# Kernel optimization log

Hardware: AMD Instinct MI355X
Metric: run time of the kernel (lower is better)

Reference implementation:

```python
import jax, jax.numpy as jnp
import numpy as np

N_NODES = 50000
N_EDGES = 800000
NUM_GRAPHS = 64
D_IN = 128
D_HID = 128
D_OUT = 1
SLOPE = 0.01  # default leaky_relu negative slope


def setup_inputs() -> dict:
    key = jax.random.key(0)
    ks = jax.random.split(key, 8)
    x = jax.random.normal(ks[0], (N_NODES, D_IN), dtype=jnp.float32)
    edge_index = jax.random.randint(ks[1], (2, N_EDGES), 0, N_NODES, dtype=jnp.int64)
    batch = jnp.sort(jax.random.randint(ks[2], (N_NODES,), 0, NUM_GRAPHS, dtype=jnp.int64))
    s_in = 1.0 / np.sqrt(D_IN)
    s_h = 1.0 / np.sqrt(D_HID)
    W0 = jax.random.uniform(ks[3], (D_IN, D_HID), jnp.float32, -s_in, s_in)
    W1 = jax.random.uniform(ks[4], (D_HID, D_HID), jnp.float32, -s_h, s_h)
    W2 = jax.random.uniform(ks[5], (D_HID, D_HID), jnp.float32, -s_h, s_h)
    Wfc1 = jax.random.uniform(ks[6], (D_HID, D_HID), jnp.float32, -s_h, s_h)
    Wfc2 = jax.random.uniform(ks[7], (D_HID, D_OUT), jnp.float32, -s_h, s_h)
    return {"x": x, "edge_index": edge_index, "batch": batch,
            "W0": W0, "W1": W1, "W2": W2, "Wfc1": Wfc1, "Wfc2": Wfc2}


def _leaky(v):
    return jnp.where(v >= 0, v, SLOPE * v)


def _gcn_layer(x, row, col, dinv, W):
    # GCNConv: h = x W; out = D^-1/2 (A+I) D^-1/2 h  (unit edge weights)
    h = x @ W
    coef = (dinv[row] * dinv[col])[:, None]            # [E,1]
    agg = jax.ops.segment_sum(h[row] * coef, col, num_segments=N_NODES)
    return agg + h * (dinv * dinv)[:, None]            # self-loop term


def reference(x, edge_index, batch, W0, W1, W2, Wfc1, Wfc2):
    row, col = edge_index[0], edge_index[1]
    # degree with self loops (edge weight 1); same for all layers
    deg = jax.ops.segment_sum(jnp.ones(N_EDGES, x.dtype), col, num_segments=N_NODES) + 1.0
    dinv = jax.lax.rsqrt(deg)
    h = x
    for W in (W0, W1, W2):
        h = _leaky(_gcn_layer(h, row, col, dinv, W))
    y = _leaky(h @ Wfc1)
    y = _leaky(y @ Wfc2)                               # [N, 1]
    # avg_pool_x(batch, y, batch): mean of y per graph id
    sums = jax.ops.segment_sum(y, batch, num_segments=NUM_GRAPHS)
    cnts = jax.ops.segment_sum(jnp.ones(N_NODES, y.dtype), batch, num_segments=NUM_GRAPHS)
    return sums / jnp.maximum(cnts, 1.0)[:, None]      # [NUM_GRAPHS, 1]
```

## Files before the change

### kernel.cpp

```cpp
#include <hip/hip_runtime.h>

#define N_NODES   50000
#define N_EDGES   800000
#define NUM_GRAPHS 64
#define D         128
#define SLOPE     0.01

__device__ __forceinline__ double dleaky(double v) { return v >= 0.0 ? v : SLOPE * v; }

__global__ void zero_kernel(int* __restrict__ p, int n) {
    int i = blockIdx.x * blockDim.x + threadIdx.x;
    if (i < n) p[i] = 0;
}

__global__ void hist_kernel(const int* __restrict__ col, int* __restrict__ hist, int E) {
    int e = blockIdx.x * blockDim.x + threadIdx.x;
    if (e < E) atomicAdd(&hist[col[e]], 1);
}

__global__ void dinv_kernel(const int* __restrict__ hist, double* __restrict__ dinvd, int n) {
    int i = blockIdx.x * blockDim.x + threadIdx.x;
    if (i < n) dinvd[i] = 1.0 / sqrt((double)hist[i] + 1.0);
}

__global__ __launch_bounds__(256) void scan1(const int* __restrict__ hist,
                                             int* __restrict__ start,
                                             int* __restrict__ bsum, int n) {
    __shared__ int tmp[256];
    const int tid = threadIdx.x;
    int base = blockIdx.x * 1024 + tid * 4;
    int v[4]; int s = 0;
#pragma unroll
    for (int i = 0; i < 4; ++i) { int idx = base + i; v[i] = (idx < n) ? hist[idx] : 0; s += v[i]; }
    tmp[tid] = s;
    __syncthreads();
    for (int off = 1; off < 256; off <<= 1) {
        int t = (tid >= off) ? tmp[tid - off] : 0;
        __syncthreads();
        tmp[tid] += t;
        __syncthreads();
    }
    int run = tmp[tid] - s;
    if (tid == 255) bsum[blockIdx.x] = tmp[255];
#pragma unroll
    for (int i = 0; i < 4; ++i) { int idx = base + i; if (idx < n) start[idx] = run; run += v[i]; }
}

__global__ __launch_bounds__(256) void scan2(int* __restrict__ bsum, int nb,
                                             int* __restrict__ start, int n) {
    __shared__ int tmp[256];
    const int tid = threadIdx.x;
    int v = (tid < nb) ? bsum[tid] : 0;
    tmp[tid] = v;
    __syncthreads();
    for (int off = 1; off < 256; off <<= 1) {
        int t = (tid >= off) ? tmp[tid - off] : 0;
        __syncthreads();
        tmp[tid] += t;
        __syncthreads();
    }
    if (tid < nb) bsum[tid] = tmp[tid] - v;
    if (tid == 255) start[n] = tmp[255];
}

__global__ __launch_bounds__(256) void scan3(int* __restrict__ start, int* __restrict__ cursor,
                                             const int* __restrict__ bsum, int n) {
    int off = bsum[blockIdx.x];
    int base = blockIdx.x * 1024 + threadIdx.x * 4;
#pragma unroll
    for (int i = 0; i < 4; ++i) {
        int j = base + i;
        if (j < n) { int v = start[j] + off; start[j] = v; cursor[j] = v; }
    }
}

__global__ void build_kernel(const int* __restrict__ row, const int* __restrict__ col,
                             int* __restrict__ cursor, int* __restrict__ srcrow, int E) {
    int e = blockIdx.x * blockDim.x + threadIdx.x;
    if (e >= E) return;
    int p = atomicAdd(&cursor[col[e]], 1);
    srcrow[p] = row[e];
}

__global__ void gbound_kernel(const int* __restrict__ batch, int* __restrict__ gstart, int n) {
    int i = blockIdx.x * blockDim.x + threadIdx.x;
    if (i >= n) return;
    int b = batch[i];
    int prev = (i == 0) ? -1 : batch[i - 1];
    for (int g = prev + 1; g <= b; ++g) gstart[g] = i;
    if (i == n - 1) {
        for (int g = b + 1; g <= NUM_GRAPHS; ++g) gstart[g] = n;
    }
}

__global__ __launch_bounds__(256, 4) void gemm128_d(const float* __restrict__ A,
                                                    const float* __restrict__ W,
                                                    float* __restrict__ C, int M, int act) {
    __shared__ double As[64][33];
    __shared__ float  Ws[32][129];
    const int tid = threadIdx.x;
    const int rg = tid >> 4;
    const int cg = tid & 15;
    const int rowBase = blockIdx.x * 64;

    double acc[4][8];
#pragma unroll
    for (int r = 0; r < 4; ++r)
#pragma unroll
        for (int j = 0; j < 8; ++j) acc[r][j] = 0.0;

    const int lr = tid >> 2;
    const int lc = (tid & 3) * 8;
    const int wr = tid & 31;
    const int wc = (tid >> 5) * 16;

    const int growA = rowBase + lr;
    const bool haveA = (growA < M);

    float4 a0 = make_float4(0.f, 0.f, 0.f, 0.f), a1 = a0;
    if (haveA) {
        const float4* src = reinterpret_cast<const float4*>(A + (size_t)growA * D + 0 + lc);
        a0 = src[0]; a1 = src[1];
    }

    for (int kc = 0; kc < 128; kc += 32) {
        *reinterpret_cast<double2*>(&As[lr][lc + 0]) = make_double2((double)a0.x, (double)a0.y);
        *reinterpret_cast<double2*>(&As[lr][lc + 2]) = make_double2((double)a0.z, (double)a0.w);
        *reinterpret_cast<double2*>(&As[lr][lc + 4]) = make_double2((double)a1.x, (double)a1.y);
        *reinterpret_cast<double2*>(&As[lr][lc + 6]) = make_double2((double)a1.z, (double)a1.w);
        {
            const float4* src = reinterpret_cast<const float4*>(W + (size_t)(kc + wr) * D + wc);
#pragma unroll
            for (int i = 0; i < 4; ++i)
                *reinterpret_cast<float4*>(&Ws[wr][wc + 4 * i]) = src[i];
        }
        __syncthreads();

        if (kc + 32 < 128 && haveA) {
            const float4* src = reinterpret_cast<const float4*>(A + (size_t)growA * D + (kc + 32) + lc);
            a0 = src[0]; a1 = src[1];
        }

#pragma unroll
        for (int k = 0; k < 32; ++k) {
            double xv0 = As[rg * 4 + 0][k];
            double xv1 = As[rg * 4 + 1][k];
            double xv2 = As[rg * 4 + 2][k];
            double xv3 = As[rg * 4 + 3][k];
            double w0 = (double)Ws[k][cg +   0];
            double w1 = (double)Ws[k][cg +  16];
            double w2 = (double)Ws[k][cg +  32];
            double w3 = (double)Ws[k][cg +  48];
            double w4 = (double)Ws[k][cg +  64];
            double w5 = (double)Ws[k][cg +  80];
            double w6 = (double)Ws[k][cg +  96];
            double w7 = (double)Ws[k][cg + 112];
            acc[0][0] = fma(xv0, w0, acc[0][0]); acc[0][1] = fma(xv0, w1, acc[0][1]);
            acc[0][2] = fma(xv0, w2, acc[0][2]); acc[0][3] = fma(xv0, w3, acc[0][3]);
            acc[0][4] = fma(xv0, w4, acc[0][4]); acc[0][5] = fma(xv0, w5, acc[0][5]);
            acc[0][6] = fma(xv0, w6, acc[0][6]); acc[0][7] = fma(xv0, w7, acc[0][7]);
            acc[1][0] = fma(xv1, w0, acc[1][0]); acc[1][1] = fma(xv1, w1, acc[1][1]);
            acc[1][2] = fma(xv1, w2, acc[1][2]); acc[1][3] = fma(xv1, w3, acc[1][3]);
            acc[1][4] = fma(xv1, w4, acc[1][4]); acc[1][5] = fma(xv1, w5, acc[1][5]);
            acc[1][6] = fma(xv1, w6, acc[1][6]); acc[1][7] = fma(xv1, w7, acc[1][7]);
            acc[2][0] = fma(xv2, w0, acc[2][0]); acc[2][1] = fma(xv2, w1, acc[2][1]);
            acc[2][2] = fma(xv2, w2, acc[2][2]); acc[2][3] = fma(xv2, w3, acc[2][3]);
            acc[2][4] = fma(xv2, w4, acc[2][4]); acc[2][5] = fma(xv2, w5, acc[2][5]);
            acc[2][6] = fma(xv2, w6, acc[2][6]); acc[2][7] = fma(xv2, w7, acc[2][7]);
            acc[3][0] = fma(xv3, w0, acc[3][0]); acc[3][1] = fma(xv3, w1, acc[3][1]);
            acc[3][2] = fma(xv3, w2, acc[3][2]); acc[3][3] = fma(xv3, w3, acc[3][3]);
            acc[3][4] = fma(xv3, w4, acc[3][4]); acc[3][5] = fma(xv3, w5, acc[3][5]);
            acc[3][6] = fma(xv3, w6, acc[3][6]); acc[3][7] = fma(xv3, w7, acc[3][7]);
        }
        __syncthreads();
    }

#pragma unroll
    for (int r = 0; r < 4; ++r) {
        int grow = rowBase + rg * 4 + r;
        if (grow < M) {
#pragma unroll
            for (int j = 0; j < 8; ++j) {
                double v = act ? dleaky(acc[r][j]) : acc[r][j];
                C[(size_t)grow * D + cg + 16 * j] = (float)v;
            }
        }
    }
}

__global__ __launch_bounds__(256) void agg_d(const float* __restrict__ h,
                                             const int* __restrict__ srcrow,
                                             const int* __restrict__ start,
                                             const double* __restrict__ dinvd,
                                             float* __restrict__ out, int n) {
    int node = (int)((blockIdx.x * blockDim.x + threadIdx.x) >> 6);
    int lane = threadIdx.x & 63;
    if (node >= n) return;
    int s = start[node], e = start[node + 1];
    double dn = dinvd[node];
    const int f = lane * 2;
    double ax = 0.0, ay = 0.0;
    int p = s;
    for (; p + 8 <= e; p += 8) {
        int r[8]; double c[8]; float2 hv[8];
#pragma unroll
        for (int i = 0; i < 8; ++i) r[i] = srcrow[p + i];
#pragma unroll
        for (int i = 0; i < 8; ++i) c[i] = dinvd[r[i]];
#pragma unroll
        for (int i = 0; i < 8; ++i)
            hv[i] = *reinterpret_cast<const float2*>(h + (size_t)r[i] * D + f);
#pragma unroll
        for (int i = 0; i < 8; ++i) {
            double cf = c[i] * dn;
            ax = fma((double)hv[i].x, cf, ax);
            ay = fma((double)hv[i].y, cf, ay);
        }
    }
    for (; p + 4 <= e; p += 4) {
        int r0 = srcrow[p + 0], r1 = srcrow[p + 1], r2 = srcrow[p + 2], r3 = srcrow[p + 3];
        double c0 = dinvd[r0], c1 = dinvd[r1], c2 = dinvd[r2], c3 = dinvd[r3];
        float2 h0 = *reinterpret_cast<const float2*>(h + (size_t)r0 * D + f);
        float2 h1 = *reinterpret_cast<const float2*>(h + (size_t)r1 * D + f);
        float2 h2 = *reinterpret_cast<const float2*>(h + (size_t)r2 * D + f);
        float2 h3 = *reinterpret_cast<const float2*>(h + (size_t)r3 * D + f);
        c0 *= dn; c1 *= dn; c2 *= dn; c3 *= dn;
        ax = fma((double)h0.x, c0, ax); ay = fma((double)h0.y, c0, ay);
        ax = fma((double)h1.x, c1, ax); ay = fma((double)h1.y, c1, ay);
        ax = fma((double)h2.x, c2, ax); ay = fma((double)h2.y, c2, ay);
        ax = fma((double)h3.x, c3, ax); ay = fma((double)h3.y, c3, ay);
    }
    for (; p < e; ++p) {
        int r = srcrow[p];
        double cf = dinvd[r] * dn;
        float2 hv = *reinterpret_cast<const float2*>(h + (size_t)r * D + f);
        ax = fma((double)hv.x, cf, ax);
        ay = fma((double)hv.y, cf, ay);
    }
    double dw = dn * dn;
    float2 hs = *reinterpret_cast<const float2*>(h + (size_t)node * D + f);
    ax = dleaky(ax + (double)hs.x * dw);
    ay = dleaky(ay + (double)hs.y * dw);
    *reinterpret_cast<float2*>(out + (size_t)node * D + f) =
        make_float2((float)ax, (float)ay);
}

__global__ __launch_bounds__(256) void fc2_d(const float* __restrict__ y,
                                             const float* __restrict__ w,
                                             double* __restrict__ s, int n) {
    int node = (int)((blockIdx.x * blockDim.x + threadIdx.x) >> 6);
    int lane = threadIdx.x & 63;
    if (node >= n) return;
    float2 yv = *reinterpret_cast<const float2*>(y + (size_t)node * D + lane * 2);
    float2 wv = *reinterpret_cast<const float2*>(w + lane * 2);
    double part = (double)yv.x * (double)wv.x + (double)yv.y * (double)wv.y;
#pragma unroll
    for (int off = 32; off > 0; off >>= 1) part += __shfl_down(part, off, 64);
    if (lane == 0) s[node] = dleaky(part);
}

__global__ __launch_bounds__(256) void pool2(const double* __restrict__ s,
                                             const int* __restrict__ gstart,
                                             float* __restrict__ out) {
    __shared__ double lsum[256];
    const int g = blockIdx.x;
    const int tid = threadIdx.x;
    const int s0 = gstart[g], s1 = gstart[g + 1];
    double sum = 0.0;
    for (int i = s0 + tid; i < s1; i += 256) sum += s[i];
    lsum[tid] = sum;
    __syncthreads();
    for (int off = 128; off > 0; off >>= 1) {
        if (tid < off) lsum[tid] += lsum[tid + off];
        __syncthreads();
    }
    if (tid == 0) {
        int cnt = s1 - s0;
        out[g] = (float)(lsum[0] / (double)(cnt > 0 ? cnt : 1));
    }
}

extern "C" void kernel_launch(void* const* d_in, const int* in_sizes, int n_in,
                              void* d_out, int out_size, void* d_ws, size_t ws_size,
                              hipStream_t stream) {
    const float* x    = (const float*)d_in[0];
    const int*   eidx = (const int*)d_in[1];
    const int*   batch= (const int*)d_in[2];
    const float* W0   = (const float*)d_in[3];
    const float* W1   = (const float*)d_in[4];
    const float* W2   = (const float*)d_in[5];
    const float* Wfc1 = (const float*)d_in[6];
    const float* Wfc2 = (const float*)d_in[7];
    float* out = (float*)d_out;

    const int* erow = eidx;
    const int* ecol = eidx + N_EDGES;

    char* ws = (char*)d_ws;
    int*    hist   = (int*)   (ws + 0);
    int*    start  = (int*)   (ws + 200064);
    int*    cursor = (int*)   (ws + 400384);
    int*    bsum   = (int*)   (ws + 600448);
    double* dinvd  = (double*)(ws + 600704);
    int*    srcrow = (int*)   (ws + 1000704);
    double* svec   = (double*)(ws + 4200704);
    float*  bufA   = (float*) (ws + 4600832);
    float*  bufB   = (float*) (ws + 30200832);
    int*    gstart = cursor;

    zero_kernel<<<(N_NODES + 255) / 256, 256, 0, stream>>>(hist, N_NODES);
    hist_kernel<<<(N_EDGES + 255) / 256, 256, 0, stream>>>(ecol, hist, N_EDGES);
    dinv_kernel<<<(N_NODES + 255) / 256, 256, 0, stream>>>(hist, dinvd, N_NODES);

    const int NB = (N_NODES + 1023) / 1024;
    scan1<<<NB, 256, 0, stream>>>(hist, start, bsum, N_NODES);
    scan2<<<1, 256, 0, stream>>>(bsum, NB, start, N_NODES);
    scan3<<<NB, 256, 0, stream>>>(start, cursor, bsum, N_NODES);

    build_kernel<<<(N_EDGES + 255) / 256, 256, 0, stream>>>(erow, ecol, cursor, srcrow, N_EDGES);
    gbound_kernel<<<(N_NODES + 255) / 256, 256, 0, stream>>>(batch, gstart, N_NODES);

    const int GEMM_GRID = (N_NODES + 63) / 64;
    const int AGG_GRID  = (N_NODES + 3) / 4;

    gemm128_d<<<GEMM_GRID, 256, 0, stream>>>(x, W0, bufA, N_NODES, 0);
    agg_d<<<AGG_GRID, 256, 0, stream>>>(bufA, srcrow, start, dinvd, bufB, N_NODES);
    gemm128_d<<<GEMM_GRID, 256, 0, stream>>>(bufB, W1, bufA, N_NODES, 0);
    agg_d<<<AGG_GRID, 256, 0, stream>>>(bufA, srcrow, start, dinvd, bufB, N_NODES);
    gemm128_d<<<GEMM_GRID, 256, 0, stream>>>(bufB, W2, bufA, N_NODES, 0);
    agg_d<<<AGG_GRID, 256, 0, stream>>>(bufA, srcrow, start, dinvd, bufB, N_NODES);
    gemm128_d<<<GEMM_GRID, 256, 0, stream>>>(bufB, Wfc1, bufA, N_NODES, 1);

    fc2_d<<<AGG_GRID, 256, 0, stream>>>(bufA, Wfc2, svec, N_NODES);
    pool2<<<NUM_GRAPHS, 256, 0, stream>>>(svec, gstart, out);
}
```

Before: 509.8 us.

## Prescale GEMM output rows by dinv to drop per-edge degree gathers in aggregation

The symmetric normalisation is factored: the GEMM epilogue multiplies each output row by dinv[row], so aggregation only sums neighbor rows and multiplies once by dinv[node] at the end. This removes the per-edge random gather of dinvd and the per-edge coefficient multiply in the memory-bound aggregation kernel. The aggregation loop also gains a 16-wide unrolled stage to keep more gathers in flight. Rounding changes slightly because the prescaled values are stored as float before summation, and the wider unroll raises register use.

```diff
diff --git a/kernel.cpp b/kernel.cpp
--- a/kernel.cpp
+++ b/kernel.cpp
@@ -95,7 +95,8 @@
 
 __global__ __launch_bounds__(256, 4) void gemm128_d(const float* __restrict__ A,
                                                     const float* __restrict__ W,
-                                                    float* __restrict__ C, int M, int act) {
+                                                    float* __restrict__ C, int M, int act,
+                                                    const double* __restrict__ scale) {
     __shared__ double As[64][33];
     __shared__ float  Ws[32][129];
     const int tid = threadIdx.x;
@@ -179,16 +180,19 @@
     for (int r = 0; r < 4; ++r) {
         int grow = rowBase + rg * 4 + r;
         if (grow < M) {
+            double sc = scale ? scale[grow] : 1.0;
 #pragma unroll
             for (int j = 0; j < 8; ++j) {
-                double v = act ? dleaky(acc[r][j]) : acc[r][j];
+                double v = acc[r][j];
+                if (act) v = dleaky(v);
+                v *= sc;
                 C[(size_t)grow * D + cg + 16 * j] = (float)v;
             }
         }
     }
 }
 
-__global__ __launch_bounds__(256) void agg_d(const float* __restrict__ h,
+__global__ __launch_bounds__(256) void agg_s(const float* __restrict__ hp,
                                              const int* __restrict__ srcrow,
                                              const int* __restrict__ start,
                                              const double* __restrict__ dinvd,
@@ -199,48 +203,36 @@
     int s = start[node], e = start[node + 1];
     double dn = dinvd[node];
     const int f = lane * 2;
+    float2 hs = *reinterpret_cast<const float2*>(hp + (size_t)node * D + f);
     double ax = 0.0, ay = 0.0;
     int p = s;
+    for (; p + 16 <= e; p += 16) {
+        int r[16]; float2 hv[16];
+#pragma unroll
+        for (int i = 0; i < 16; ++i) r[i] = srcrow[p + i];
+#pragma unroll
+        for (int i = 0; i < 16; ++i)
+            hv[i] = *reinterpret_cast<const float2*>(hp + (size_t)r[i] * D + f);
+#pragma unroll
+        for (int i = 0; i < 16; ++i) { ax += (double)hv[i].x; ay += (double)hv[i].y; }
+    }
     for (; p + 8 <= e; p += 8) {
-        int r[8]; double c[8]; float2 hv[8];
+        int r[8]; float2 hv[8];
 #pragma unroll
         for (int i = 0; i < 8; ++i) r[i] = srcrow[p + i];
 #pragma unroll
-        for (int i = 0; i < 8; ++i) c[i] = dinvd[r[i]];
-#pragma unroll
         for (int i = 0; i < 8; ++i)
-            hv[i] = *reinterpret_cast<const float2*>(h + (size_t)r[i] * D + f);
-#pragma unroll
-        for (int i = 0; i < 8; ++i) {
-            double cf = c[i] * dn;
-            ax = fma((double)hv[i].x, cf, ax);
-            ay = fma((double)hv[i].y, cf, ay);
-        }
-    }
-    for (; p + 4 <= e; p += 4) {
-        int r0 = srcrow[p + 0], r1 = srcrow[p + 1], r2 = srcrow[p + 2], r3 = srcrow[p + 3];
-        double c0 = dinvd[r0], c1 = dinvd[r1], c2 = dinvd[r2], c3 = dinvd[r3];
-        float2 h0 = *reinterpret_cast<const float2*>(h + (size_t)r0 * D + f);
-        float2 h1 = *reinterpret_cast<const float2*>(h + (size_t)r1 * D + f);
-        float2 h2 = *reinterpret_cast<const float2*>(h + (size_t)r2 * D + f);
-        float2 h3 = *reinterpret_cast<const float2*>(h + (size_t)r3 * D + f);
-        c0 *= dn; c1 *= dn; c2 *= dn; c3 *= dn;
-        ax = fma((double)h0.x, c0, ax); ay = fma((double)h0.y, c0, ay);
-        ax = fma((double)h1.x, c1, ax); ay = fma((double)h1.y, c1, ay);
-        ax = fma((double)h2.x, c2, ax); ay = fma((double)h2.y, c2, ay);
-        ax = fma((double)h3.x, c3, ax); ay = fma((double)h3.y, c3, ay);
+            hv[i] = *reinterpret_cast<const float2*>(hp + (size_t)r[i] * D + f);
+#pragma unroll
+        for (int i = 0; i < 8; ++i) { ax += (double)hv[i].x; ay += (double)hv[i].y; }
     }
     for (; p < e; ++p) {
         int r = srcrow[p];
-        double cf = dinvd[r] * dn;
-        float2 hv = *reinterpret_cast<const float2*>(h + (size_t)r * D + f);
-        ax = fma((double)hv.x, cf, ax);
-        ay = fma((double)hv.y, cf, ay);
-    }
-    double dw = dn * dn;
-    float2 hs = *reinterpret_cast<const float2*>(h + (size_t)node * D + f);
-    ax = dleaky(ax + (double)hs.x * dw);
-    ay = dleaky(ay + (double)hs.y * dw);
+        float2 hv = *reinterpret_cast<const float2*>(hp + (size_t)r * D + f);
+        ax += (double)hv.x; ay += (double)hv.y;
+    }
+    ax = dleaky((ax + (double)hs.x) * dn);
+    ay = dleaky((ay + (double)hs.y) * dn);
     *reinterpret_cast<float2*>(out + (size_t)node * D + f) =
         make_float2((float)ax, (float)ay);
 }
@@ -323,13 +315,13 @@
     const int GEMM_GRID = (N_NODES + 63) / 64;
     const int AGG_GRID  = (N_NODES + 3) / 4;
 
-    gemm128_d<<<GEMM_GRID, 256, 0, stream>>>(x, W0, bufA, N_NODES, 0);
-    agg_d<<<AGG_GRID, 256, 0, stream>>>(bufA, srcrow, start, dinvd, bufB, N_NODES);
-    gemm128_d<<<GEMM_GRID, 256, 0, stream>>>(bufB, W1, bufA, N_NODES, 0);
-    agg_d<<<AGG_GRID, 256, 0, stream>>>(bufA, srcrow, start, dinvd, bufB, N_NODES);
-    gemm128_d<<<GEMM_GRID, 256, 0, stream>>>(bufB, W2, bufA, N_NODES, 0);
-    agg_d<<<AGG_GRID, 256, 0, stream>>>(bufA, srcrow, start, dinvd, bufB, N_NODES);
-    gemm128_d<<<GEMM_GRID, 256, 0, stream>>>(bufB, Wfc1, bufA, N_NODES, 1);
+    gemm128_d<<<GEMM_GRID, 256, 0, stream>>>(x, W0, bufA, N_NODES, 0, dinvd);
+    agg_s<<<AGG_GRID, 256, 0, stream>>>(bufA, srcrow, start, dinvd, bufB, N_NODES);
+    gemm128_d<<<GEMM_GRID, 256, 0, stream>>>(bufB, W1, bufA, N_NODES, 0, dinvd);
+    agg_s<<<AGG_GRID, 256, 0, stream>>>(bufA, srcrow, start, dinvd, bufB, N_NODES);
+    gemm128_d<<<GEMM_GRID, 256, 0, stream>>>(bufB, W2, bufA, N_NODES, 0, dinvd);
+    agg_s<<<AGG_GRID, 256, 0, stream>>>(bufA, srcrow, start, dinvd, bufB, N_NODES);
+    gemm128_d<<<GEMM_GRID, 256, 0, stream>>>(bufB, Wfc1, bufA, N_NODES, 1, (const double*)nullptr);
 
     fc2_d<<<AGG_GRID, 256, 0, stream>>>(bufA, Wfc2, svec, N_NODES);
     pool2<<<NUM_GRAPHS, 256, 0, stream>>>(svec, gstart, out);
```

Measured after the change: 500.3 us. No clear change (-1.9%).
